# Kernel tuning notes

Hardware: AMD Instinct MI355X
Metric: run time of the kernel (lower is better)

## Reference

```python
import jax, jax.numpy as jnp
import numpy as np

B, N, D = 32, 512, 256
ITERATION_STEPS = 2


def setup_inputs() -> dict:
    key = jax.random.key(0)
    ks = jax.random.split(key, 20)
    node = jax.random.normal(ks[0], (B, N, D), dtype=jnp.float32)
    node_mask = jnp.ones((B, N), dtype=jnp.int32)
    graphs = [(jax.random.uniform(ks[1 + i], (B, N, N)) < 0.05).astype(jnp.int32)
              for i in range(6)]
    s = 0.02
    params = {
        'w_nw': jax.random.normal(ks[8], (D, 1)) * s,
        'b_nw': jnp.zeros((1,), jnp.float32),
        'w_self': jax.random.normal(ks[9], (D, D)) * s,
        'b_self': jnp.zeros((D,), jnp.float32),
        'w_arg1': jax.random.normal(ks[10], (D, D)) * s,
        'w_arg2': jax.random.normal(ks[11], (D, D)) * s,
        'w_arg3': jax.random.normal(ks[12], (D, D)) * s,
        'w_arg4': jax.random.normal(ks[13], (D, D)) * s,
        'w_punct': jax.random.normal(ks[14], (D, D)) * s,
        'w_punct_re': jax.random.normal(ks[15], (D, D)) * s,
    }
    return {'node': node, 'node_mask': node_mask,
            'arg_graph_1': graphs[0], 'arg_graph_2': graphs[1],
            'arg_graph_3': graphs[2], 'arg_graph_4': graphs[3],
            'punct_graph': graphs[4], 'punct_graph_re': graphs[5],
            **params}


def reference(node, node_mask, arg_graph_1, arg_graph_2, arg_graph_3, arg_graph_4,
              punct_graph, punct_graph_re,
              w_nw, b_nw, w_self, b_self,
              w_arg1, w_arg2, w_arg3, w_arg4, w_punct, w_punct_re):
    n = node.shape[1]
    diag = jnp.eye(n, dtype=node_mask.dtype)  # [N,N]
    # dd_graph: pairwise valid mask with zeroed diagonal, [B,N,N]
    dd = node_mask[:, None, :] * node_mask[:, :, None] * (1 - diag)
    G = jnp.stack([arg_graph_1, arg_graph_2, arg_graph_3, arg_graph_4,
                   punct_graph, punct_graph_re], 0) * dd[None]  # [6,B,N,N]
    Gf = G.astype(node.dtype)
    # neighbor count over all 6 edge types; replace 0 by 1 to avoid div-by-zero
    nn_num = Gf.sum(axis=(0, -1))  # [B,N]
    nn_num = jnp.where(nn_num >= 1, nn_num, jnp.ones_like(nn_num))
    W = jnp.stack([w_arg1, w_arg2, w_arg3, w_arg4, w_punct, w_punct_re], 0)  # [6,D,D]

    all_weight = []
    for _ in range(ITERATION_STEPS):
        # (1) node relatedness measure
        d_node_weight = jax.nn.sigmoid(node @ w_nw + b_nw)[..., 0]  # [B,N]
        all_weight.append(d_node_weight)
        self_node_info = node @ w_self + b_self  # [B,N,D]
        # (2) message propagation: per edge type k, project then aggregate
        proj = jnp.einsum('bnd,kde->kbne', node, W)            # [6,B,N,D]
        masked_w = d_node_weight[None, :, None, :] * Gf        # [6,B,N,N]
        agg = jnp.einsum('kbmn,kbne->bme', masked_w, proj)     # [B,N,D]
        # (3) update
        node = jax.nn.relu(self_node_info + agg / nn_num[..., None])
    return node, jnp.stack(all_weight, axis=1)  # [B,N,D], [B,steps,N]
```

## Files before the change

### kernel.cpp

```cpp
#include <hip/hip_runtime.h>

#define Bb 32
#define Nn 512
#define Dd 256
#define KC 1792

typedef __bf16 bf16x8 __attribute__((ext_vector_type(8)));
typedef float  f32x4  __attribute__((ext_vector_type(4)));
typedef unsigned short u16;

__device__ __forceinline__ u16 f2bf(float x){
  union { float f; unsigned u; } c; c.f = x;
  unsigned u = c.u;
  u += 0x7FFFu + ((u >> 16) & 1u);
  return (u16)(u >> 16);
}

__global__ __launch_bounds__(256) void k_prep(
    const float* __restrict__ wself,
    const float* __restrict__ w0, const float* __restrict__ w1,
    const float* __restrict__ w2, const float* __restrict__ w3,
    const float* __restrict__ w4, const float* __restrict__ w5,
    u16* __restrict__ wcatT){
  int e = blockIdx.x;
  const float* Ws[7] = {wself, w0, w1, w2, w3, w4, w5};
  for (int c = threadIdx.x; c < KC; c += 256){
    int g = c >> 8, j = c & 255;
    wcatT[(size_t)e*KC + c] = f2bf(Ws[g][j*Dd + e]);
  }
}

__global__ __launch_bounds__(512) void k_mask(
    const int* __restrict__ mask, unsigned* __restrict__ Mp){
  int t = threadIdx.x;
  int b = t >> 4, w = t & 15;
  const int4* mp = (const int4*)(mask + (size_t)b * Nn + w * 32);
  unsigned v = 0;
  #pragma unroll
  for (int j = 0; j < 8; ++j){
    int4 x = mp[j];
    v |= ((unsigned)x.x << (j * 4)) | ((unsigned)x.y << (j * 4 + 1)) |
         ((unsigned)x.z << (j * 4 + 2)) | ((unsigned)x.w << (j * 4 + 3));
  }
  Mp[t] = v;
}

__global__ __launch_bounds__(256) void k_pack(
    const int* __restrict__ g0, const int* __restrict__ g1,
    const int* __restrict__ g2, const int* __restrict__ g3,
    const int* __restrict__ g4, const int* __restrict__ g5,
    const int* __restrict__ mask, const unsigned* __restrict__ Mp,
    unsigned* __restrict__ Gp, float* __restrict__ rs){
  int t = blockIdx.x * 256 + threadIdx.x;
  int w = t & 15, r = t >> 4;
  int b = r >> 9, m = r & 511;
  unsigned keep = Mp[b * 16 + w] & ~(((m >> 5) == w) ? (1u << (m & 31)) : 0u);
  const int* gs[6] = {g0, g1, g2, g3, g4, g5};
  int stot = 0;
  #pragma unroll
  for (int k = 0; k < 6; ++k){
    const int4* gp = (const int4*)(gs[k] + (size_t)r * Nn + w * 32);
    unsigned v = 0;
    #pragma unroll
    for (int j = 0; j < 8; ++j){
      int4 x = gp[j];
      v |= ((unsigned)x.x << (j * 4)) | ((unsigned)x.y << (j * 4 + 1)) |
           ((unsigned)x.z << (j * 4 + 2)) | ((unsigned)x.w << (j * 4 + 3));
    }
    v &= keep;
    stot += __popc(v);
    Gp[((size_t)k * Bb * Nn + r) * 16 + w] = v;
  }
  stot += __shfl_xor(stot, 1);
  stot += __shfl_xor(stot, 2);
  stot += __shfl_xor(stot, 4);
  stot += __shfl_xor(stot, 8);
  if (w == 0)
    rs[r] = mask[r] ? 1.0f / (float)(stot < 1 ? 1 : stot) : 0.0f;
}

__global__ __launch_bounds__(256) void k_dw(
    const float* __restrict__ node, const int* __restrict__ mask,
    const float* __restrict__ wnw, const float* __restrict__ bnw,
    float* __restrict__ aw_out,
    u16* __restrict__ Z, u16* __restrict__ XT){
  __shared__ float tile[32][268];
  __shared__ float dws[32];
  int b = blockIdx.x >> 4, n0 = (blockIdx.x & 15) << 5;
  int t = threadIdx.x;
  int row = t >> 3, seg = t & 7;
  const float* src = node + ((size_t)(b * Nn + n0 + row)) * Dd + seg * 32;
  u16* zn = Z + ((size_t)(b * Nn + n0 + row)) * KC + seg * 32;
  #pragma unroll
  for (int c = 0; c < 8; ++c){
    float4 v = ((const float4*)src)[c];
    tile[row][seg * 32 + c * 4 + 0] = v.x;
    tile[row][seg * 32 + c * 4 + 1] = v.y;
    tile[row][seg * 32 + c * 4 + 2] = v.z;
    tile[row][seg * 32 + c * 4 + 3] = v.w;
    ushort4 h;
    h.x = f2bf(v.x); h.y = f2bf(v.y); h.z = f2bf(v.z); h.w = f2bf(v.w);
    ((ushort4*)zn)[c] = h;
  }
  __syncthreads();
  float s = 0.f;
  #pragma unroll
  for (int c = 0; c < 32; ++c) s += tile[row][seg * 32 + c] * wnw[seg * 32 + c];
  s += __shfl_xor(s, 1); s += __shfl_xor(s, 2); s += __shfl_xor(s, 4);
  if (seg == 0){
    float dw = 1.f / (1.f + expf(-(s + bnw[0])));
    aw_out[b * (2 * Nn) + n0 + row] = dw;
    dws[row] = mask[b * Nn + n0 + row] ? dw : 0.f;
  }
  __syncthreads();
  #pragma unroll
  for (int p = 0; p < 4; ++p){
    int d = p * 64 + (t >> 2);
    int j0 = (t & 3) * 8;
    union { u16 h[8]; uint4 v; } pk;
    #pragma unroll
    for (int jj = 0; jj < 8; ++jj)
      pk.h[jj] = f2bf(dws[j0 + jj] * tile[j0 + jj][d]);
    *(uint4*)(XT + ((size_t)(b * Dd + d)) * Nn + n0 + j0) = pk.v;
  }
}

__global__ __launch_bounds__(256) void k_agg(
    const unsigned* __restrict__ Gp,
    const u16* __restrict__ XT, const float* __restrict__ rs,
    u16* __restrict__ Z){
  int mt = blockIdx.x, b = blockIdx.y, kg = blockIdx.z;
  int m0 = mt * 64;
  const unsigned* Gr = Gp + ((size_t)kg * Bb * Nn + b * Nn + m0) * 16;
  const u16* Xb = XT + (size_t)b * Dd * Nn;
  __shared__ u16 As[64 * 72];
  __shared__ u16 Bs[256 * 72];
  int t = threadIdx.x, lane = t & 63, wn = t >> 6;
  int arow = t >> 2, aq = t & 3;
  unsigned wpre[8];
  #pragma unroll
  for (int ks = 0; ks < 8; ++ks)
    wpre[ks] = Gr[arow * 16 + ks * 2 + (aq >> 1)];

  f32x4 acc[4][4];
  #pragma unroll
  for (int i = 0; i < 4; ++i)
    #pragma unroll
    for (int q = 0; q < 4; ++q) acc[i][q] = (f32x4){0.f, 0.f, 0.f, 0.f};

  for (int ks = 0; ks < 8; ++ks){
    int k0 = ks * 64;
    {
      unsigned bits = (wpre[ks] >> ((aq & 1) * 16)) & 0xFFFFu;
      union { u16 h[16]; uint4 v[2]; } pk;
      #pragma unroll
      for (int c = 0; c < 16; ++c)
        pk.h[c] = ((bits >> c) & 1u) ? 0x3F80 : 0;
      *(uint4*)&As[arow * 72 + aq * 16]     = pk.v[0];
      *(uint4*)&As[arow * 72 + aq * 16 + 8] = pk.v[1];
    }
    #pragma unroll
    for (int p = 0; p < 8; ++p){
      int rowb = p * 32 + (t >> 3);
      *(uint4*)&Bs[rowb * 72 + (t & 7) * 8] =
          *(const uint4*)(Xb + (size_t)rowb * Nn + k0 + (t & 7) * 8);
    }
    __syncthreads();
    #pragma unroll
    for (int kk = 0; kk < 2; ++kk){
      bf16x8 av[4], bv[4];
      #pragma unroll
      for (int i = 0; i < 4; ++i)
        av[i] = *(const bf16x8*)&As[(i * 16 + (lane & 15)) * 72 + kk * 32 + (lane >> 4) * 8];
      #pragma unroll
      for (int q = 0; q < 4; ++q)
        bv[q] = *(const bf16x8*)&Bs[(wn * 64 + q * 16 + (lane & 15)) * 72 + kk * 32 + (lane >> 4) * 8];
      #pragma unroll
      for (int i = 0; i < 4; ++i)
        #pragma unroll
        for (int q = 0; q < 4; ++q)
          acc[i][q] = __builtin_amdgcn_mfma_f32_16x16x32_bf16(av[i], bv[q], acc[i][q], 0, 0, 0);
    }
    __syncthreads();
  }
  int kgcol = 256 + kg * 256 + wn * 64;
  #pragma unroll
  for (int i = 0; i < 4; ++i){
    #pragma unroll
    for (int r = 0; r < 4; ++r){
      int mg = m0 + i * 16 + (lane >> 4) * 4 + r;
      float sc = rs[b * Nn + mg];
      u16* zp = Z + ((size_t)(b * Nn + mg)) * KC + kgcol + (lane & 15);
      #pragma unroll
      for (int q = 0; q < 4; ++q)
        zp[q * 16] = f2bf(acc[i][q][r] * sc);
    }
  }
}

__global__ __launch_bounds__(256) void k_upd(
    const u16* __restrict__ Z, const u16* __restrict__ wcatT,
    const float* __restrict__ bself, float* __restrict__ outp){
  int n0 = blockIdx.x * 128, m0 = blockIdx.y * 128;
  __shared__ u16 As[128 * 72];
  __shared__ u16 Bs[128 * 72];
  int t = threadIdx.x, lane = t & 63, wid = t >> 6;
  int wm = wid >> 1, wn = wid & 1;
  f32x4 acc[4][4];
  #pragma unroll
  for (int i = 0; i < 4; ++i)
    #pragma unroll
    for (int q = 0; q < 4; ++q) acc[i][q] = (f32x4){0.f, 0.f, 0.f, 0.f};

  for (int ks = 0; ks < 28; ++ks){
    int k0 = ks * 64;
    #pragma unroll
    for (int p = 0; p < 4; ++p){
      int row = p * 32 + (t >> 3);
      *(uint4*)&As[row * 72 + (t & 7) * 8] =
          *(const uint4*)(Z + ((size_t)(m0 + row)) * KC + k0 + (t & 7) * 8);
      *(uint4*)&Bs[row * 72 + (t & 7) * 8] =
          *(const uint4*)(wcatT + ((size_t)(n0 + row)) * KC + k0 + (t & 7) * 8);
    }
    __syncthreads();
    #pragma unroll
    for (int kk = 0; kk < 2; ++kk){
      bf16x8 av[4], bv[4];
      #pragma unroll
      for (int i = 0; i < 4; ++i)
        av[i] = *(const bf16x8*)&As[(wm * 64 + i * 16 + (lane & 15)) * 72 + kk * 32 + (lane >> 4) * 8];
      #pragma unroll
      for (int q = 0; q < 4; ++q)
        bv[q] = *(const bf16x8*)&Bs[(wn * 64 + q * 16 + (lane & 15)) * 72 + kk * 32 + (lane >> 4) * 8];
      #pragma unroll
      for (int i = 0; i < 4; ++i)
        #pragma unroll
        for (int q = 0; q < 4; ++q)
          acc[i][q] = __builtin_amdgcn_mfma_f32_16x16x32_bf16(av[i], bv[q], acc[i][q], 0, 0, 0);
    }
    __syncthreads();
  }
  #pragma unroll
  for (int i = 0; i < 4; ++i){
    #pragma unroll
    for (int r = 0; r < 4; ++r){
      int mg = m0 + wm * 64 + i * 16 + (lane >> 4) * 4 + r;
      #pragma unroll
      for (int q = 0; q < 4; ++q){
        int e = n0 + wn * 64 + q * 16 + (lane & 15);
        float v = acc[i][q][r] + bself[e];
        outp[(size_t)mg * Dd + e] = v > 0.f ? v : 0.f;
      }
    }
  }
}

extern "C" void kernel_launch(void* const* d_in, const int* in_sizes, int n_in,
                              void* d_out, int out_size, void* d_ws, size_t ws_size,
                              hipStream_t stream){
  (void)in_sizes; (void)n_in; (void)out_size; (void)ws_size;
  const float* node  = (const float*)d_in[0];
  const int*   mask  = (const int*)d_in[1];
  const int*   g[6];
  for (int i = 0; i < 6; ++i) g[i] = (const int*)d_in[2 + i];
  const float* wnw   = (const float*)d_in[8];
  const float* bnw   = (const float*)d_in[9];
  const float* wself = (const float*)d_in[10];
  const float* bself = (const float*)d_in[11];
  const float* W[6];
  for (int i = 0; i < 6; ++i) W[i] = (const float*)d_in[12 + i];

  float* out_node = (float*)d_out;
  float* out_aw   = out_node + (size_t)Bb * Nn * Dd;

  char* ws = (char*)d_ws;
  u16*      wcatT = (u16*)(ws);
  float*    rs    = (float*)(ws + 917504);
  unsigned* Mp    = (unsigned*)(ws + 983040);
  unsigned* Gp    = (unsigned*)(ws + 1048576);
  u16*      XT    = (u16*)(ws + 7340032);
  u16*      Z     = (u16*)(ws + 15728640);

  k_prep<<<256, 256, 0, stream>>>(wself, W[0], W[1], W[2], W[3], W[4], W[5], wcatT);
  k_mask<<<1, 512, 0, stream>>>(mask, Mp);
  k_pack<<<1024, 256, 0, stream>>>(g[0], g[1], g[2], g[3], g[4], g[5], mask, Mp, Gp, rs);

  for (int t = 0; t < 2; ++t){
    const float* nsrc = (t == 0) ? node : out_node;
    k_dw<<<512, 256, 0, stream>>>(nsrc, mask, wnw, bnw, out_aw + t * Nn, Z, XT);
    k_agg<<<dim3(8, 32, 6), 256, 0, stream>>>(Gp, XT, rs, Z);
    k_upd<<<dim3(2, 128), 256, 0, stream>>>(Z, wcatT, bself, out_node);
  }
}
```

Baseline: 263.2 us.

## Stage adjacency loads through LDS with double-buffered global_load_lds in pack kernel

The graph bit-packing kernel now has each 256-thread block process 16 rows. It streams each row's six int32 adjacency slices into shared memory with asynchronous global-to-LDS loads, double-buffered so the load of the next row overlaps packing of the current one. Only 96 threads do the bit packing and popcount reduction from LDS, and the per-row reciprocal count is written by one thread. This aims to raise memory-level parallelism on the dominant int32 graph read, at the cost of barriers, idle threads during compute, and hand-written waitcnt logic.

```diff
diff --git a/kernel.cpp b/kernel.cpp
--- a/kernel.cpp
+++ b/kernel.cpp
@@ -8,6 +8,9 @@
 typedef __bf16 bf16x8 __attribute__((ext_vector_type(8)));
 typedef float  f32x4  __attribute__((ext_vector_type(4)));
 typedef unsigned short u16;
+
+typedef const __attribute__((address_space(1))) void cgv_t;
+typedef __attribute__((address_space(3))) void lv_t;
 
 __device__ __forceinline__ u16 f2bf(float x){
   union { float f; unsigned u; } c; c.f = x;
@@ -45,38 +48,91 @@
   Mp[t] = v;
 }
 
+__device__ __forceinline__ void gl16(const int* src, int* dst){
+  __builtin_amdgcn_global_load_lds((cgv_t*)src, (lv_t*)dst, 16, 0, 0);
+}
+
 __global__ __launch_bounds__(256) void k_pack(
     const int* __restrict__ g0, const int* __restrict__ g1,
     const int* __restrict__ g2, const int* __restrict__ g3,
     const int* __restrict__ g4, const int* __restrict__ g5,
     const int* __restrict__ mask, const unsigned* __restrict__ Mp,
     unsigned* __restrict__ Gp, float* __restrict__ rs){
-  int t = blockIdx.x * 256 + threadIdx.x;
-  int w = t & 15, r = t >> 4;
-  int b = r >> 9, m = r & 511;
-  unsigned keep = Mp[b * 16 + w] & ~(((m >> 5) == w) ? (1u << (m & 31)) : 0u);
-  const int* gs[6] = {g0, g1, g2, g3, g4, g5};
-  int stot = 0;
-  #pragma unroll
-  for (int k = 0; k < 6; ++k){
-    const int4* gp = (const int4*)(gs[k] + (size_t)r * Nn + w * 32);
-    unsigned v = 0;
-    #pragma unroll
-    for (int j = 0; j < 8; ++j){
-      int4 x = gp[j];
-      v |= ((unsigned)x.x << (j * 4)) | ((unsigned)x.y << (j * 4 + 1)) |
-           ((unsigned)x.z << (j * 4 + 2)) | ((unsigned)x.w << (j * 4 + 3));
-    }
-    v &= keep;
-    stot += __popc(v);
-    Gp[((size_t)k * Bb * Nn + r) * 16 + w] = v;
-  }
-  stot += __shfl_xor(stot, 1);
-  stot += __shfl_xor(stot, 2);
-  stot += __shfl_xor(stot, 4);
-  stot += __shfl_xor(stot, 8);
-  if (w == 0)
-    rs[r] = mask[r] ? 1.0f / (float)(stot < 1 ? 1 : stot) : 0.0f;
+  __shared__ int buf[2][3072];
+  __shared__ int red[2];
+  int t = threadIdx.x, lane = t & 63, wv = t >> 6;
+  int R = blockIdx.x * 16, b = R >> 9;
+
+  int c0 = wv * 3, c1 = c0 + 1, c2 = c0 + 2;
+  const int* p0 = g0;
+  const int* p1 = g0; const int* p2 = g0;
+  {
+    int k0 = c0 >> 1, k1 = c1 >> 1, k2 = c2 >> 1;
+    p0 = (k0==1)?g1:p0; p0 = (k0==2)?g2:p0; p0 = (k0==3)?g3:p0; p0 = (k0==4)?g4:p0; p0 = (k0==5)?g5:p0;
+    p1 = (k1==1)?g1:p1; p1 = (k1==2)?g2:p1; p1 = (k1==3)?g3:p1; p1 = (k1==4)?g4:p1; p1 = (k1==5)?g5:p1;
+    p2 = (k2==1)?g1:p2; p2 = (k2==2)?g2:p2; p2 = (k2==3)?g3:p2; p2 = (k2==4)?g4:p2; p2 = (k2==5)?g5:p2;
+  }
+  const int* s0 = p0 + (size_t)R * Nn + (c0 & 1) * 256 + lane * 4;
+  const int* s1 = p1 + (size_t)R * Nn + (c1 & 1) * 256 + lane * 4;
+  const int* s2 = p2 + (size_t)R * Nn + (c2 & 1) * 256 + lane * 4;
+  int* d0[2] = {&buf[0][c0 * 256], &buf[1][c0 * 256]};
+  int* d1[2] = {&buf[0][c1 * 256], &buf[1][c1 * 256]};
+  int* d2[2] = {&buf[0][c2 * 256], &buf[1][c2 * 256]};
+
+  int kk = t >> 4, ww = t & 15;
+  unsigned keepw = (t < 96) ? Mp[b * 16 + ww] : 0u;
+
+#define STAGE(B) { gl16(s0, d0[B]); gl16(s1, d1[B]); gl16(s2, d2[B]); \
+                   s0 += Nn; s1 += Nn; s2 += Nn; }
+
+  auto consume = [&](const int* cb, int r){
+    if (t < 96){
+      int m = r & 511;
+      unsigned keep = keepw & ~(((m >> 5) == ww) ? (1u << (m & 31)) : 0u);
+      const int4* p = (const int4*)(cb + kk * 512 + ww * 32);
+      unsigned v = 0;
+      #pragma unroll
+      for (int j = 0; j < 8; ++j){
+        int4 x = p[j];
+        v |= ((unsigned)x.x << (j * 4)) | ((unsigned)x.y << (j * 4 + 1)) |
+             ((unsigned)x.z << (j * 4 + 2)) | ((unsigned)x.w << (j * 4 + 3));
+      }
+      v &= keep;
+      Gp[((size_t)kk * (Bb * Nn) + r) * 16 + ww] = v;
+      int s = __popc(v);
+      s += __shfl_xor(s, 1); s += __shfl_xor(s, 2); s += __shfl_xor(s, 4);
+      s += __shfl_xor(s, 8); s += __shfl_xor(s, 16);
+      if (wv == 0) s += __shfl_xor(s, 32);
+      if (lane == 0) red[wv] = s;
+    }
+  };
+  auto rs_row = [&](int r){
+    if (t == 0){
+      int s = red[0] + red[1];
+      rs[r] = mask[r] ? 1.0f / (float)(s < 1 ? 1 : s) : 0.0f;
+    }
+  };
+
+  STAGE(0); STAGE(1);
+  for (int p = 0; p < 8; ++p){
+    int r0 = R + 2 * p, r1 = r0 + 1;
+    asm volatile("s_waitcnt vmcnt(3)" ::: "memory");
+    __builtin_amdgcn_s_barrier();
+    __builtin_amdgcn_sched_barrier(0);
+    consume(buf[0], r0);
+    __builtin_amdgcn_s_barrier();
+    rs_row(r0);
+    if (p < 7) STAGE(0);
+    if (p < 7) { asm volatile("s_waitcnt vmcnt(3)" ::: "memory"); }
+    else       { asm volatile("s_waitcnt vmcnt(0)" ::: "memory"); }
+    __builtin_amdgcn_s_barrier();
+    __builtin_amdgcn_sched_barrier(0);
+    consume(buf[1], r1);
+    __builtin_amdgcn_s_barrier();
+    rs_row(r1);
+    if (p < 7) STAGE(1);
+  }
+#undef STAGE
 }
 
 __global__ __launch_bounds__(256) void k_dw(
```

Result: faster. 254.0 us (-3.5%).
